# Kernel optimization log

Measured on AMD Instinct MI355X. Metric: run time of the kernel, lower is better.

Reference implementation:

```python
import jax, jax.numpy as jnp
import numpy as np

E, DE, DN, N = 640000, 128, 128, 50000

def setup_inputs() -> dict:
    key = jax.random.key(0)
    k0, k1, k2, k3 = jax.random.split(key, 4)
    edge_features = jax.random.normal(k0, (E, DE), dtype=jnp.float32)
    edge_index = jax.random.randint(k1, (2, E), 0, N, dtype=jnp.int64)
    W1 = jax.random.normal(k2, (2 * DE, DE), dtype=jnp.float32) * 0.02
    b1 = jnp.zeros((DE,), dtype=jnp.float32)
    W2 = jax.random.normal(k3, (DE, DN), dtype=jnp.float32) * 0.02
    b2 = jnp.zeros((DN,), dtype=jnp.float32)
    return {"edge_features": edge_features, "W1": W1, "b1": b1,
            "W2": W2, "b2": b2, "edge_index": edge_index, "num_nodes": N}

def _segment_mean(feats, seg_ids, num_segments):
    # scatter-sum then divide by count; zero vector for empty segments
    s = jax.ops.segment_sum(feats, seg_ids, num_segments=num_segments)
    c = jax.ops.segment_sum(jnp.ones((feats.shape[0],), feats.dtype), seg_ids,
                            num_segments=num_segments)
    return s / jnp.maximum(c, 1.0)[:, None]

def reference(edge_features, W1, b1, W2, b2, edge_index, num_nodes):
    src = edge_index[0]
    dst = edge_index[1]
    subject_feat = _segment_mean(edge_features, src, num_nodes)  # [N, DE]
    object_feat = _segment_mean(edge_features, dst, num_nodes)   # [N, DE]
    combined = jnp.concatenate([subject_feat, object_feat], axis=-1)  # [N, 2*DE]
    h = jax.nn.relu(combined @ W1 + b1)
    attention = jax.nn.sigmoid(h @ W2 + b2)  # [N, DN]
    return attention
```

## Files before the change

### kernel.cpp

```cpp
#include <hip/hip_runtime.h>

static constexpr int N = 50000;
static constexpr int E = 640000;
static constexpr int D = 128;
static constexpr int NPB = 8;
static constexpr int CAP = 64;

static constexpr int C     = 64;
static constexpr int CHUNK = E / C;
static constexpr int NR    = 4;
static constexpr int RANGE = N / NR;


__global__ __launch_bounds__(256) void hist_kernel(
    const int* __restrict__ eidx,
    unsigned char* __restrict__ counts_s, unsigned char* __restrict__ counts_d)
{
    __shared__ unsigned int h[RANGE];
    const int c   = blockIdx.x;
    const int lo  = blockIdx.y * RANGE;
    const int dir = blockIdx.z;
    const int t   = threadIdx.x;

    for (int i = t; i < RANGE; i += 256) h[i] = 0;
    __syncthreads();

    const int* __restrict__ src = eidx + dir * E + c * CHUNK;
    for (int i = t; i < CHUNK; i += 256) {
        int n = src[i] - lo;
        if ((unsigned)n < (unsigned)RANGE) atomicAdd(&h[n], 1u);
    }
    __syncthreads();

    unsigned char* out = (dir ? counts_d : counts_s) + (size_t)c * N + lo;
    unsigned int* out4 = (unsigned int*)out;
    for (int i = t; i < RANGE / 4; i += 256) {
        unsigned int v = (h[4 * i] & 255u)
                       | ((h[4 * i + 1] & 255u) << 8)
                       | ((h[4 * i + 2] & 255u) << 16)
                       | ((h[4 * i + 3] & 255u) << 24);
        out4[i] = v;
    }
}

__global__ __launch_bounds__(256) void scan_kernel(
    unsigned char* __restrict__ counts_s, unsigned char* __restrict__ counts_d,
    int* __restrict__ deg_s, int* __restrict__ deg_d)
{
    const int node = blockIdx.x * 256 + threadIdx.x;
    if (node >= N) return;
    unsigned char* cnt = blockIdx.y ? counts_d : counts_s;
    int* deg = blockIdx.y ? deg_d : deg_s;

    int acc = 0;
    for (int c = 0; c < C; ++c) {
        const size_t idx = (size_t)c * N + node;
        int v = cnt[idx];
        cnt[idx] = (unsigned char)acc;
        acc += v;
    }
    deg[node] = acc;
}

__global__ __launch_bounds__(256) void scatter_kernel(
    const int* __restrict__ eidx,
    const unsigned char* __restrict__ counts_s, const unsigned char* __restrict__ counts_d,
    int* __restrict__ ids_s, int* __restrict__ ids_d)
{
    __shared__ unsigned int h[RANGE];
    const int c   = blockIdx.x;
    const int lo  = blockIdx.y * RANGE;
    const int dir = blockIdx.z;
    const int t   = threadIdx.x;

    for (int i = t; i < RANGE; i += 256) h[i] = 0;
    __syncthreads();

    const int* __restrict__ src = eidx + dir * E + c * CHUNK;
    const unsigned char* __restrict__ offs = (dir ? counts_d : counts_s) + (size_t)c * N;
    int* __restrict__ ids = dir ? ids_d : ids_s;

    for (int i = t; i < CHUNK; i += 256) {
        const int node = src[i];
        const int n = node - lo;
        if ((unsigned)n < (unsigned)RANGE) {
            const int rank = (int)atomicAdd(&h[n], 1u);
            const int slot = (int)offs[node] + rank;
            if (slot < CAP) ids[((size_t)node << 6) + slot] = c * CHUNK + i;
        }
    }
}

__global__ __launch_bounds__(128) void fused_kernel(
    const float* __restrict__ feat,
    const int* __restrict__ ids_s, const int* __restrict__ deg_s,
    const int* __restrict__ ids_d, const int* __restrict__ deg_d,
    const float* __restrict__ W1,
    const float* __restrict__ b1,
    const float* __restrict__ W2,
    const float* __restrict__ b2,
    float* __restrict__ out)
{
    __shared__ float4 m4[NPB][2 * D / 4];
    __shared__ float4 h4[NPB][D / 4];

    const int j = threadIdx.x;
    const int base = blockIdx.x * NPB;
    const float4* __restrict__ feat4 = (const float4*)feat;

    const int sub  = j >> 5;
    const int lane = j & 31;

    for (int g = 0; g < 4; ++g) {
        const int w    = (g << 2) | sub;
        const int n    = w >> 1;
        const int dir  = w & 1;
        const int node = base + n;
        const int* __restrict__ ids = dir ? ids_d : ids_s;
        const int* __restrict__ deg = dir ? deg_d : deg_s;
        const int st = node << 6;
        int dg = deg[node];
        dg = dg < CAP ? dg : CAP;

        float4 a = make_float4(0.f, 0.f, 0.f, 0.f);
        int i = 0;
        for (; i + 4 <= dg; i += 4) {
            const int e0 = ids[st + i + 0];
            const int e1 = ids[st + i + 1];
            const int e2 = ids[st + i + 2];
            const int e3 = ids[st + i + 3];
            float4 v0 = feat4[(size_t)e0 * (D / 4) + lane];
            float4 v1 = feat4[(size_t)e1 * (D / 4) + lane];
            float4 v2 = feat4[(size_t)e2 * (D / 4) + lane];
            float4 v3 = feat4[(size_t)e3 * (D / 4) + lane];
            a.x += (v0.x + v1.x) + (v2.x + v3.x);
            a.y += (v0.y + v1.y) + (v2.y + v3.y);
            a.z += (v0.z + v1.z) + (v2.z + v3.z);
            a.w += (v0.w + v1.w) + (v2.w + v3.w);
        }
        for (; i < dg; ++i) {
            float4 v = feat4[(size_t)ids[st + i] * (D / 4) + lane];
            a.x += v.x; a.y += v.y; a.z += v.z; a.w += v.w;
        }
        const float inv = 1.0f / (float)(dg > 0 ? dg : 1);
        m4[n][dir * (D / 4) + lane] =
            make_float4(a.x * inv, a.y * inv, a.z * inv, a.w * inv);
    }
    __syncthreads();

    float acc[NPB];
    const float bb1 = b1[j];
    #pragma unroll
    for (int n = 0; n < NPB; ++n) acc[n] = bb1;

    for (int k4 = 0; k4 < 2 * D / 4; ++k4) {
        const int k = k4 * 4;
        float w0 = W1[(k + 0) * D + j];
        float w1v = W1[(k + 1) * D + j];
        float w2v = W1[(k + 2) * D + j];
        float w3v = W1[(k + 3) * D + j];
        #pragma unroll
        for (int n = 0; n < NPB; ++n) {
            float4 mv = m4[n][k4];
            acc[n] = fmaf(mv.x, w0, acc[n]);
            acc[n] = fmaf(mv.y, w1v, acc[n]);
            acc[n] = fmaf(mv.z, w2v, acc[n]);
            acc[n] = fmaf(mv.w, w3v, acc[n]);
        }
    }
    #pragma unroll
    for (int n = 0; n < NPB; ++n)
        ((float*)&h4[n][0])[j] = fmaxf(acc[n], 0.0f);
    __syncthreads();

    float o[NPB];
    const float bb2 = b2[j];
    #pragma unroll
    for (int n = 0; n < NPB; ++n) o[n] = bb2;

    for (int k4 = 0; k4 < D / 4; ++k4) {
        const int k = k4 * 4;
        float w0 = W2[(k + 0) * D + j];
        float w1v = W2[(k + 1) * D + j];
        float w2v = W2[(k + 2) * D + j];
        float w3v = W2[(k + 3) * D + j];
        #pragma unroll
        for (int n = 0; n < NPB; ++n) {
            float4 hv = h4[n][k4];
            o[n] = fmaf(hv.x, w0, o[n]);
            o[n] = fmaf(hv.y, w1v, o[n]);
            o[n] = fmaf(hv.z, w2v, o[n]);
            o[n] = fmaf(hv.w, w3v, o[n]);
        }
    }
    #pragma unroll
    for (int n = 0; n < NPB; ++n)
        out[(size_t)(base + n) * D + j] = 1.0f / (1.0f + __expf(-o[n]));
}

extern "C" void kernel_launch(void* const* d_in, const int* in_sizes, int n_in,
                              void* d_out, int out_size, void* d_ws, size_t ws_size,
                              hipStream_t stream) {
    const float* feat = (const float*)d_in[0];
    const float* W1   = (const float*)d_in[1];
    const float* b1   = (const float*)d_in[2];
    const float* W2   = (const float*)d_in[3];
    const float* b2   = (const float*)d_in[4];
    const int*   eidx = (const int*)d_in[5];
    float* out = (float*)d_out;

    int* deg_s = (int*)d_ws;
    int* deg_d = deg_s + N;
    int* ids_s = deg_d + N;
    int* ids_d = ids_s + N * CAP;
    unsigned char* counts_s = (unsigned char*)(ids_d + N * CAP);
    unsigned char* counts_d = counts_s + (size_t)C * N;

    hist_kernel<<<dim3(C, NR, 2), 256, 0, stream>>>(eidx, counts_s, counts_d);
    scan_kernel<<<dim3((N + 255) / 256, 2), 256, 0, stream>>>(
        counts_s, counts_d, deg_s, deg_d);
    scatter_kernel<<<dim3(C, NR, 2), 256, 0, stream>>>(
        eidx, counts_s, counts_d, ids_s, ids_d);
    fused_kernel<<<N / NPB, 128, 0, stream>>>(
        feat, ids_s, deg_s, ids_d, deg_d,
        W1, b1, W2, b2, out);
}
```

Before: 630.7 us.

## Widen fused block to 16 nodes and 256 threads, unroll gather by eight

The fused gather-MLP kernel now handles 16 nodes per block with 256 threads. The two 128-thread halves each compute the MLP for 8 nodes, so each block reads the W1 and W2 weights once for twice as many nodes. The edge-feature gather loop is unrolled to 8 outstanding loads to raise memory-level parallelism. The histogram and scatter passes use 32 edge chunks instead of 64, which means fewer blocks and a smaller count array, at the cost of less parallelism in those passes.

After: 671.0 us. +6.4%, slower.

```diff
diff --git a/kernel.cpp b/kernel.cpp
--- a/kernel.cpp
+++ b/kernel.cpp
@@ -3,10 +3,10 @@
 static constexpr int N = 50000;
 static constexpr int E = 640000;
 static constexpr int D = 128;
-static constexpr int NPB = 8;
+static constexpr int NPB = 16;
 static constexpr int CAP = 64;
 
-static constexpr int C     = 64;
+static constexpr int C     = 32;
 static constexpr int CHUNK = E / C;
 static constexpr int NR    = 4;
 static constexpr int RANGE = N / NR;
@@ -91,7 +91,7 @@
     }
 }
 
-__global__ __launch_bounds__(128) void fused_kernel(
+__global__ __launch_bounds__(256) void fused_kernel(
     const float* __restrict__ feat,
     const int* __restrict__ ids_s, const int* __restrict__ deg_s,
     const int* __restrict__ ids_d, const int* __restrict__ deg_d,
@@ -104,15 +104,15 @@
     __shared__ float4 m4[NPB][2 * D / 4];
     __shared__ float4 h4[NPB][D / 4];
 
-    const int j = threadIdx.x;
+    const int t    = threadIdx.x;
     const int base = blockIdx.x * NPB;
     const float4* __restrict__ feat4 = (const float4*)feat;
 
-    const int sub  = j >> 5;
-    const int lane = j & 31;
+    const int sub  = t >> 5;
+    const int lane = t & 31;
 
     for (int g = 0; g < 4; ++g) {
-        const int w    = (g << 2) | sub;
+        const int w    = (g << 3) | sub;
         const int n    = w >> 1;
         const int dir  = w & 1;
         const int node = base + n;
@@ -124,7 +124,29 @@
 
         float4 a = make_float4(0.f, 0.f, 0.f, 0.f);
         int i = 0;
-        for (; i + 4 <= dg; i += 4) {
+        for (; i + 8 <= dg; i += 8) {
+            const int e0 = ids[st + i + 0];
+            const int e1 = ids[st + i + 1];
+            const int e2 = ids[st + i + 2];
+            const int e3 = ids[st + i + 3];
+            const int e4 = ids[st + i + 4];
+            const int e5 = ids[st + i + 5];
+            const int e6 = ids[st + i + 6];
+            const int e7 = ids[st + i + 7];
+            float4 v0 = feat4[(size_t)e0 * (D / 4) + lane];
+            float4 v1 = feat4[(size_t)e1 * (D / 4) + lane];
+            float4 v2 = feat4[(size_t)e2 * (D / 4) + lane];
+            float4 v3 = feat4[(size_t)e3 * (D / 4) + lane];
+            float4 v4 = feat4[(size_t)e4 * (D / 4) + lane];
+            float4 v5 = feat4[(size_t)e5 * (D / 4) + lane];
+            float4 v6 = feat4[(size_t)e6 * (D / 4) + lane];
+            float4 v7 = feat4[(size_t)e7 * (D / 4) + lane];
+            a.x += ((v0.x + v1.x) + (v2.x + v3.x)) + ((v4.x + v5.x) + (v6.x + v7.x));
+            a.y += ((v0.y + v1.y) + (v2.y + v3.y)) + ((v4.y + v5.y) + (v6.y + v7.y));
+            a.z += ((v0.z + v1.z) + (v2.z + v3.z)) + ((v4.z + v5.z) + (v6.z + v7.z));
+            a.w += ((v0.w + v1.w) + (v2.w + v3.w)) + ((v4.w + v5.w) + (v6.w + v7.w));
+        }
+        if (i + 4 <= dg) {
             const int e0 = ids[st + i + 0];
             const int e1 = ids[st + i + 1];
             const int e2 = ids[st + i + 2];
@@ -137,6 +159,7 @@
             a.y += (v0.y + v1.y) + (v2.y + v3.y);
             a.z += (v0.z + v1.z) + (v2.z + v3.z);
             a.w += (v0.w + v1.w) + (v2.w + v3.w);
+            i += 4;
         }
         for (; i < dg; ++i) {
             float4 v = feat4[(size_t)ids[st + i] * (D / 4) + lane];
@@ -148,54 +171,57 @@
     }
     __syncthreads();
 
-    float acc[NPB];
+    const int j  = t & 127;
+    const int nb = (t >> 7) * (NPB / 2);
+
+    float acc[NPB / 2];
     const float bb1 = b1[j];
     #pragma unroll
-    for (int n = 0; n < NPB; ++n) acc[n] = bb1;
+    for (int nn = 0; nn < NPB / 2; ++nn) acc[nn] = bb1;
 
     for (int k4 = 0; k4 < 2 * D / 4; ++k4) {
         const int k = k4 * 4;
-        float w0 = W1[(k + 0) * D + j];
+        float w0  = W1[(k + 0) * D + j];
         float w1v = W1[(k + 1) * D + j];
         float w2v = W1[(k + 2) * D + j];
         float w3v = W1[(k + 3) * D + j];
         #pragma unroll
-        for (int n = 0; n < NPB; ++n) {
-            float4 mv = m4[n][k4];
-            acc[n] = fmaf(mv.x, w0, acc[n]);
-            acc[n] = fmaf(mv.y, w1v, acc[n]);
-            acc[n] = fmaf(mv.z, w2v, acc[n]);
-            acc[n] = fmaf(mv.w, w3v, acc[n]);
-        }
-    }
-    #pragma unroll
-    for (int n = 0; n < NPB; ++n)
-        ((float*)&h4[n][0])[j] = fmaxf(acc[n], 0.0f);
-    __syncthreads();
-
-    float o[NPB];
+        for (int nn = 0; nn < NPB / 2; ++nn) {
+            float4 mv = m4[nb + nn][k4];
+            acc[nn] = fmaf(mv.x, w0,  acc[nn]);
+            acc[nn] = fmaf(mv.y, w1v, acc[nn]);
+            acc[nn] = fmaf(mv.z, w2v, acc[nn]);
+            acc[nn] = fmaf(mv.w, w3v, acc[nn]);
+        }
+    }
+    #pragma unroll
+    for (int nn = 0; nn < NPB / 2; ++nn)
+        ((float*)&h4[nb + nn][0])[j] = fmaxf(acc[nn], 0.0f);
+    __syncthreads();
+
+    float o[NPB / 2];
     const float bb2 = b2[j];
     #pragma unroll
-    for (int n = 0; n < NPB; ++n) o[n] = bb2;
+    for (int nn = 0; nn < NPB / 2; ++nn) o[nn] = bb2;
 
     for (int k4 = 0; k4 < D / 4; ++k4) {
         const int k = k4 * 4;
-        float w0 = W2[(k + 0) * D + j];
+        float w0  = W2[(k + 0) * D + j];
         float w1v = W2[(k + 1) * D + j];
         float w2v = W2[(k + 2) * D + j];
         float w3v = W2[(k + 3) * D + j];
         #pragma unroll
-        for (int n = 0; n < NPB; ++n) {
-            float4 hv = h4[n][k4];
-            o[n] = fmaf(hv.x, w0, o[n]);
-            o[n] = fmaf(hv.y, w1v, o[n]);
-            o[n] = fmaf(hv.z, w2v, o[n]);
-            o[n] = fmaf(hv.w, w3v, o[n]);
-        }
-    }
-    #pragma unroll
-    for (int n = 0; n < NPB; ++n)
-        out[(size_t)(base + n) * D + j] = 1.0f / (1.0f + __expf(-o[n]));
+        for (int nn = 0; nn < NPB / 2; ++nn) {
+            float4 hv = h4[nb + nn][k4];
+            o[nn] = fmaf(hv.x, w0,  o[nn]);
+            o[nn] = fmaf(hv.y, w1v, o[nn]);
+            o[nn] = fmaf(hv.z, w2v, o[nn]);
+            o[nn] = fmaf(hv.w, w3v, o[nn]);
+        }
+    }
+    #pragma unroll
+    for (int nn = 0; nn < NPB / 2; ++nn)
+        out[(size_t)(base + nb + nn) * D + j] = 1.0f / (1.0f + __expf(-o[nn]));
 }
 
 extern "C" void kernel_launch(void* const* d_in, const int* in_sizes, int n_in,
@@ -221,7 +247,7 @@
         counts_s, counts_d, deg_s, deg_d);
     scatter_kernel<<<dim3(C, NR, 2), 256, 0, stream>>>(
         eidx, counts_s, counts_d, ids_s, ids_d);
-    fused_kernel<<<N / NPB, 128, 0, stream>>>(
+    fused_kernel<<<N / NPB, 256, 0, stream>>>(
         feat, ids_s, deg_s, ids_d, deg_d,
         W1, b1, W2, b2, out);
 }
```
